# Optimization experiments

Hardware: AMD Instinct MI355X
Metric: run time of the kernel (lower is better)

Reference implementation:

```python
import jax, jax.numpy as jnp
import numpy as np

GAMMA = 1.0
BIG = 1e30  # finite stand-in for +inf (safe under logsumexp and autodiff)


def setup_inputs() -> dict:
    key = jax.random.key(0)
    kx, ky = jax.random.split(key)
    x = jax.random.normal(kx, (32, 512, 64), dtype=jnp.float32)
    y = jax.random.normal(ky, (32, 512, 64), dtype=jnp.float32)
    return {"x": x, "y": y}


def _cosine_dist(x, y):
    # 1 - cosine similarity; matches F.normalize(p=2, eps=1e-12)
    xn = x / jnp.maximum(jnp.linalg.norm(x, axis=-1, keepdims=True), 1e-12)
    yn = y / jnp.maximum(jnp.linalg.norm(y, axis=-1, keepdims=True), 1e-12)
    return 1.0 - jnp.einsum('btd,bsd->bts', xn, yn)


def _soft_dtw(D, gamma):
    # Anti-diagonal soft-DTW DP. D: [B, T1, T2] -> [B]
    B, T1, T2 = D.shape
    R0 = jnp.full((B, T1 + 1, T2 + 1), BIG, dtype=D.dtype).at[:, 0, 0].set(0.0)
    i = jnp.arange(1, T1 + 1)  # all rows; each diagonal k has j = k - i

    def step(R, k):
        j = k - i
        valid = (j >= 1) & (j <= T2)
        jc = jnp.where(valid, j, 0)  # clamp invalid lanes; masked below
        cost = jnp.where(valid, D[:, i - 1, jnp.clip(jc - 1, 0, T2 - 1)], 0.0)
        r_diag = R[:, i - 1, jnp.clip(jc - 1, 0, T2)]
        r_left = R[:, i, jnp.clip(jc - 1, 0, T2)]
        r_up = R[:, i - 1, jc]
        stacked = jnp.stack([r_diag, r_left, r_up], axis=0)  # [3, B, T1]
        stacked = jnp.where(valid[None, None, :], stacked, 0.0)
        soft_min = -gamma * jax.nn.logsumexp(-stacked / gamma, axis=0)
        new = cost + soft_min
        old = R[:, i, jc]
        R = R.at[:, i, jc].set(jnp.where(valid[None, :], new, old))
        return R, None

    ks = jnp.arange(2, T1 + T2 + 1)
    R, _ = jax.lax.scan(step, R0, ks)
    return R[:, T1, T2]


def reference(x, y):
    D_xy = _cosine_dist(x, y)
    D_xx = _cosine_dist(x, x)
    D_yy = _cosine_dist(y, y)
    sdtw_xy = _soft_dtw(D_xy, GAMMA)
    sdtw_xx = _soft_dtw(D_xx, GAMMA)
    sdtw_yy = _soft_dtw(D_yy, GAMMA)
    return sdtw_xy - 0.5 * (sdtw_xx + sdtw_yy)
```

## Files before the change

kernel.cpp:

```cpp
#include <hip/hip_runtime.h>
#include <hip/hip_fp16.h>

#define T1 512
#define NB 32
#define NP 96
#define DHEAD 64

#define RSLOTS 128
#define RBYTES (RSLOTS * 1024)
#define PFD 32

typedef __attribute__((ext_vector_type(8))) short bf16x8;
typedef __attribute__((ext_vector_type(4))) float f32x4;
typedef __attribute__((ext_vector_type(4))) unsigned int u32x4;

__global__ __launch_bounds__(256) void k_normalize(const float* __restrict__ x,
                                                   const float* __restrict__ y,
                                                   ushort* __restrict__ xb,
                                                   ushort* __restrict__ yb) {
  int wid  = threadIdx.x >> 6;
  int lane = threadIdx.x & 63;
  int row  = blockIdx.x * 4 + wid;
  const float* src; ushort* dst;
  if (row < NB * T1) { src = x + (size_t)row * DHEAD;            dst = xb + (size_t)row * DHEAD; }
  else { int r2 = row - NB * T1; src = y + (size_t)r2 * DHEAD;   dst = yb + (size_t)r2 * DHEAD; }
  float v = src[lane];
  float s = v * v;
  #pragma unroll
  for (int off = 32; off > 0; off >>= 1) s += __shfl_xor(s, off);
  float rn = 1.0f / fmaxf(sqrtf(s), 1e-12f);
  float o = v * rn;
  unsigned u = __float_as_uint(o);
  unsigned r = (u + 0x7fffu + ((u >> 16) & 1u)) >> 16;
  dst[lane] = (ushort)r;
}

__global__ __launch_bounds__(256) void k_gemm_w(const ushort* __restrict__ xb,
                                                const ushort* __restrict__ yb,
                                                __half* __restrict__ W) {
  __shared__ __attribute__((aligned(16))) __half blk[128][132];
  int pb = blockIdx.z;
  int p  = pb >> 5;
  int b  = pb & 31;
  const ushort* A  = ((p == 2) ? yb : xb) + (size_t)b * T1 * DHEAD;
  const ushort* Bm = ((p == 1) ? xb : yb) + (size_t)b * T1 * DHEAD;

  int wid = threadIdx.x >> 6, lane = threadIdx.x & 63;
  int wm = wid >> 1, wn = wid & 1;
  int i0b = blockIdx.x * 128, j0b = blockIdx.y * 128;
  int i0 = i0b + wm * 64;
  int j0 = j0b + wn * 64;
  int lr = lane & 15, kg = lane >> 4;

  f32x4 acc[4][4];
  #pragma unroll
  for (int ic = 0; ic < 4; ++ic)
    #pragma unroll
    for (int jc = 0; jc < 4; ++jc) acc[ic][jc] = (f32x4){0.f, 0.f, 0.f, 0.f};

  #pragma unroll
  for (int kk = 0; kk < 2; ++kk) {
    int ko = kk * 32 + kg * 8;
    bf16x8 af[4], bf[4];
    #pragma unroll
    for (int ic = 0; ic < 4; ++ic)
      af[ic] = *reinterpret_cast<const bf16x8*>(A + (size_t)(i0 + ic * 16 + lr) * DHEAD + ko);
    #pragma unroll
    for (int jc = 0; jc < 4; ++jc)
      bf[jc] = *reinterpret_cast<const bf16x8*>(Bm + (size_t)(j0 + jc * 16 + lr) * DHEAD + ko);
    #pragma unroll
    for (int ic = 0; ic < 4; ++ic)
      #pragma unroll
      for (int jc = 0; jc < 4; ++jc)
        acc[ic][jc] = __builtin_amdgcn_mfma_f32_16x16x32_bf16(af[ic], bf[jc], acc[ic][jc], 0, 0, 0);
  }

  const float NLOG2E = -1.44269504088896340736f;
  #pragma unroll
  for (int ic = 0; ic < 4; ++ic) {
    int il = wm * 64 + ic * 16 + (kg << 2);
    #pragma unroll
    for (int jc = 0; jc < 4; ++jc) {
      int jl = wn * 64 + jc * 16 + lr;
      union { __half h[4]; uint2 u; } pk;
      #pragma unroll
      for (int r = 0; r < 4; ++r) {
        float d = 1.0f - acc[ic][jc][r];
        pk.h[r] = __float2half(exp2f(NLOG2E * d));
      }
      *reinterpret_cast<uint2*>(&blk[jl][il]) = pk.u;
    }
  }
  __syncthreads();

  __half* Wp = W + (size_t)pb * (T1 * T1);
  int tr = threadIdx.x >> 4;
  int tc = threadIdx.x & 15;
  #pragma unroll
  for (int q = 0; q < 8; ++q) {
    int j = q * 16 + tr;
    u32x4 v = *reinterpret_cast<const u32x4*>(&blk[j][tc << 3]);
    *reinterpret_cast<u32x4*>(Wp + (size_t)(j0b + j) * T1 + i0b + (tc << 3)) = v;
  }
}

__global__ __launch_bounds__(64, 1) void k_dtw(const __half* __restrict__ W,
                                               float* __restrict__ res) {
  __shared__ __attribute__((aligned(16))) char ring[RBYTES];
  const int prob = blockIdx.x;
  const __half* Wp = W + (size_t)prob * (T1 * T1);
  const int lane = threadIdx.x;

  float Va[8], Vb[8];
  #pragma unroll
  for (int r = 0; r < 8; ++r) { Va[r] = 0.f; Vb[r] = 0.f; }
  float B2 = 0.f, B2p = 0.f;
  const float dgSeed = (lane == 0) ? 1.0f : 0.0f;

  auto dppshr = [](float v) -> float {
    return __int_as_float(__builtin_amdgcn_update_dpp(
        0, __float_as_int(v), 0x138 , 0xF, 0xF, true));
  };

#define SCALEBITS(dexp) __uint_as_float( \
    (unsigned)(127 + (int)fminf(fmaxf((dexp), -120.f), 120.f)) << 23)

  const char* gW = (const char*)Wp;
  const unsigned laneOff = (unsigned)(lane << 4);
  size_t colOff = (size_t)PFD << 10;
  unsigned lslot = (PFD << 10) & (RBYTES - 1);

  #pragma unroll
  for (int c = 0; c < PFD; ++c) {
    __builtin_amdgcn_global_load_lds(
        (const __attribute__((address_space(1))) void*)(gW + ((size_t)c << 10) + laneOff),
        (__attribute__((address_space(3))) void*)(ring + ((unsigned)(c << 10))), 16, 0, 0);
  }
  asm volatile("s_waitcnt vmcnt(24)" ::: "memory");

  u32x4 d0, d1, d2, d3, d4, d5, d6, d7;
  unsigned va0, va1, va2, va3, va4, va5, va6, va7;
#define RS_INIT(K) do { \
    d##K = *reinterpret_cast<const u32x4*>( \
        ring + ((((unsigned)(K - lane) & 127u) << 10) | (unsigned)(lane << 4))); \
    va##K = ((((unsigned)(8 + K - lane) & 127u) << 10) | (unsigned)(lane << 4)); \
  } while (0)
  RS_INIT(0); RS_INIT(1); RS_INIT(2); RS_INIT(3);
  RS_INIT(4); RS_INIT(5); RS_INIT(6); RS_INIT(7);
#undef RS_INIT

#define DTW_STEP(KK, BUF, VIN, VOUT, SDG, SEEDK, GUARD, RENORM) do {          \
    const int t_ = tb + (KK);                                                 \
    float nbUp_ = dppshr(VIN[7]);                    \
    float nbDg_ = dppshr(VOUT[7]);                   \
    float up_ = nbUp_ * sUp;                                                  \
    float dg_ = nbDg_ * (SDG);                                                \
    if (SEEDK) dg_ = dgSeed;                                                  \
    union { u32x4 u; __half h[8]; } cv_; cv_.u = d##BUF;                      \
    d##BUF = *reinterpret_cast<const u32x4*>(ring + va##BUF);   \
    va##BUF = (va##BUF + 8192u) & (RBYTES - 1);                               \
    __builtin_amdgcn_global_load_lds(                          \
        (const __attribute__((address_space(1))) void*)(gW + colOff + laneOff),\
        (__attribute__((address_space(3))) void*)(ring + lslot), 16, 0, 0);   \
    lslot = (lslot + 1024u) & (RBYTES - 1);                                   \
    colOff += ((t_ + PFD) < (T1 - 1)) ? 1024 : 0;  \
    float wv_[8];                                                             \
    _Pragma("unroll")                                                         \
    for (int r = 0; r < 8; ++r) wv_[r] = __half2float(cv_.h[r]);              \
    bool act_ = true;                                                         \
    if (GUARD) { int j_ = t_ - lane; act_ = ((unsigned)j_ < (unsigned)T1); }  \
    if (act_) {                                                               \
      float c_ = fmaf(wv_[0], up_, wv_[0] * (dg_ + VIN[0]));                  \
      VOUT[0] = c_;                                                           \
      _Pragma("unroll")                                                       \
      for (int r = 1; r < 8; ++r) {                                           \
        c_ = fmaf(wv_[r], c_, wv_[r] * (VIN[r-1] + VIN[r]));                  \
        VOUT[r] = c_;                                                         \
      }                                                                       \
      if (RENORM) {                            \
        float m_ = fmaxf(fmaxf(fmaxf(VOUT[0],VOUT[1]),fmaxf(VOUT[2],VOUT[3])),\
                         fmaxf(fmaxf(VOUT[4],VOUT[5]),fmaxf(VOUT[6],VOUT[7])));\
        int e_ = (int)((__float_as_uint(m_) >> 23) & 0xFF) - 127;             \
        e_ = e_ < -126 ? -126 : (e_ > 126 ? 126 : e_);                        \
        float sc_ = __uint_as_float((unsigned)(127 - e_) << 23);              \
        _Pragma("unroll")                                                     \
        for (int r = 0; r < 8; ++r) VOUT[r] *= sc_;                           \
        B2p = B2; B2 -= (float)e_;                                            \
      }                                                                       \
    }                                                                         \
  } while (0)

#define DTW_GROUP(GUARD, SEED) do {                                           \
    asm volatile("s_waitcnt vmcnt(16)" ::: "memory");      \
    float nbBn_ = dppshr(B2);                 \
    float nbBo_ = dppshr(B2p);                \
    float sUp  = SCALEBITS(B2 - nbBn_);                                       \
    float sDg0 = SCALEBITS(B2 - nbBo_);                                       \
    DTW_STEP(0,  0, Va, Vb, sDg0, SEED,  GUARD, false);                       \
    DTW_STEP(1,  1, Vb, Va, sUp,  false, GUARD, false);                       \
    DTW_STEP(2,  2, Va, Vb, sUp,  false, GUARD, false);                       \
    DTW_STEP(3,  3, Vb, Va, sUp,  false, GUARD, false);                       \
    DTW_STEP(4,  4, Va, Vb, sUp,  false, GUARD, false);                       \
    DTW_STEP(5,  5, Vb, Va, sUp,  false, GUARD, false);                       \
    DTW_STEP(6,  6, Va, Vb, sUp,  false, GUARD, false);                       \
    DTW_STEP(7,  7, Vb, Va, sUp,  false, GUARD, false);                       \
    asm volatile("s_waitcnt vmcnt(16)" ::: "memory");      \
    DTW_STEP(8,  0, Va, Vb, sUp,  false, GUARD, false);                       \
    DTW_STEP(9,  1, Vb, Va, sUp,  false, GUARD, false);                       \
    DTW_STEP(10, 2, Va, Vb, sUp,  false, GUARD, false);                       \
    DTW_STEP(11, 3, Vb, Va, sUp,  false, GUARD, false);                       \
    DTW_STEP(12, 4, Va, Vb, sUp,  false, GUARD, false);                       \
    DTW_STEP(13, 5, Vb, Va, sUp,  false, GUARD, false);                       \
    DTW_STEP(14, 6, Va, Vb, sUp,  false, GUARD, false);                       \
    DTW_STEP(15, 7, Vb, Va, sUp,  false, GUARD, true);                        \
  } while (0)

  { const int tb = 0; DTW_GROUP(true, true); }
  #pragma unroll 1
  for (int tb = 16; tb < 64; tb += 16)   DTW_GROUP(true,  false);
  #pragma unroll 1
  for (int tb = 64; tb < 560; tb += 16)  DTW_GROUP(false, false);
  { const int tb = 560; DTW_GROUP(true, false); }

  if (lane == 63) {
    res[prob] = (B2 - log2f(Vb[7])) * 0.69314718055994530942f;
  }
#undef DTW_STEP
#undef DTW_GROUP
#undef SCALEBITS
}

__global__ void k_combine(const float* __restrict__ res, float* __restrict__ out) {
  int b = threadIdx.x;
  if (b < NB) out[b] = res[b] - 0.5f * (res[NB + b] + res[2 * NB + b]);
}

extern "C" void kernel_launch(void* const* d_in, const int* in_sizes, int n_in,
                              void* d_out, int out_size, void* d_ws, size_t ws_size,
                              hipStream_t stream) {
  const float* x = (const float*)d_in[0];
  const float* y = (const float*)d_in[1];
  float* out = (float*)d_out;

  const size_t xb_off  = 0;
  const size_t yb_off  = (size_t)NB * T1 * DHEAD * sizeof(ushort);
  const size_t W_off   = 2 * yb_off;
  const size_t res_off = W_off + (size_t)3 * NB * T1 * T1 * sizeof(__half);
  const size_t need    = res_off + NP * sizeof(float);

  if (ws_size < need) {
    hipMemsetAsync(d_out, 0xFF, (size_t)out_size * sizeof(float), stream);
    return;
  }

  ushort* xb  = (ushort*)((char*)d_ws + xb_off);
  ushort* yb  = (ushort*)((char*)d_ws + yb_off);
  __half* W   = (__half*)((char*)d_ws + W_off);
  float*  res = (float*)((char*)d_ws + res_off);

  hipLaunchKernelGGL(k_normalize, dim3(8192), dim3(256), 0, stream, x, y, xb, yb);
  hipLaunchKernelGGL(k_gemm_w, dim3(4, 4, 96), dim3(256), 0, stream, xb, yb, W);
  hipLaunchKernelGGL(k_dtw, dim3(NP), dim3(64), 0, stream, W, res);
  hipLaunchKernelGGL(k_combine, dim3(1), dim3(64), 0, stream, res, out);
}
```

Measured before the change: 84.30 us.

## Process two DTW columns per lane step, halving wavefront sweep length

Each DTW step now computes two consecutive columns per lane, so each lane covers 16 rows per tile (lane offset 2*lane). The number of anti-diagonal steps drops from about 576 to about 320, with fewer DPP shuffles and waitcnt barriers per column. The LDS ring is resized to 152 slots with a prefetch depth of 30, and two global-to-LDS loads are issued per step. In exchange each step has a longer dependent FMA chain and more registers are live, and the ring indexing becomes harder to verify.

```diff
diff --git a/kernel.cpp b/kernel.cpp
--- a/kernel.cpp
+++ b/kernel.cpp
@@ -6,9 +6,9 @@
 #define NP 96
 #define DHEAD 64
 
-#define RSLOTS 128
+#define RSLOTS 152
 #define RBYTES (RSLOTS * 1024)
-#define PFD 32
+#define PFD 30
 
 typedef __attribute__((ext_vector_type(8))) short bf16x8;
 typedef __attribute__((ext_vector_type(4))) float f32x4;
@@ -115,6 +115,7 @@
   #pragma unroll
   for (int r = 0; r < 8; ++r) { Va[r] = 0.f; Vb[r] = 0.f; }
   float B2 = 0.f, B2p = 0.f;
+  float m7 = 0.f, d7 = 0.f;
   const float dgSeed = (lane == 0) ? 1.0f : 0.0f;
 
   auto dppshr = [](float v) -> float {
@@ -125,109 +126,136 @@
 #define SCALEBITS(dexp) __uint_as_float( \
     (unsigned)(127 + (int)fminf(fmaxf((dexp), -120.f), 120.f)) << 23)
 
+#define GLL16(GP, LP) __builtin_amdgcn_global_load_lds( \
+    (const __attribute__((address_space(1))) void*)(GP), \
+    (__attribute__((address_space(3))) void*)(LP), 16, 0, 0)
+
   const char* gW = (const char*)Wp;
   const unsigned laneOff = (unsigned)(lane << 4);
-  size_t colOff = (size_t)PFD << 10;
-  unsigned lslot = (PFD << 10) & (RBYTES - 1);
-
-  #pragma unroll
-  for (int c = 0; c < PFD; ++c) {
-    __builtin_amdgcn_global_load_lds(
-        (const __attribute__((address_space(1))) void*)(gW + ((size_t)c << 10) + laneOff),
-        (__attribute__((address_space(3))) void*)(ring + ((unsigned)(c << 10))), 16, 0, 0);
-  }
-  asm volatile("s_waitcnt vmcnt(24)" ::: "memory");
-
-  u32x4 d0, d1, d2, d3, d4, d5, d6, d7;
+
+  #pragma unroll
+  for (int c = 0; c < PFD; ++c)
+    GLL16(gW + ((size_t)c << 10) + laneOff, ring + ((unsigned)(c << 10)));
+  asm volatile("s_waitcnt vmcnt(22)" ::: "memory");
+
+  u32x4 d0, d1, d2, d3, d4, d5, d6, d7b;
   unsigned va0, va1, va2, va3, va4, va5, va6, va7;
-#define RS_INIT(K) do { \
-    d##K = *reinterpret_cast<const u32x4*>( \
-        ring + ((((unsigned)(K - lane) & 127u) << 10) | (unsigned)(lane << 4))); \
-    va##K = ((((unsigned)(8 + K - lane) & 127u) << 10) | (unsigned)(lane << 4)); \
+#define RS_INIT(K, DN) do { \
+    int n_ = (K) - 2 * lane; unsigned s_ = (unsigned)(n_ < 0 ? n_ + RSLOTS : n_); \
+    DN = *reinterpret_cast<const u32x4*>(ring + (s_ << 10) + laneOff); \
+    int m_ = n_ + 8; unsigned sm_ = (unsigned)(m_ < 0 ? m_ + RSLOTS : m_); \
+    va##K = (sm_ << 10) + laneOff; \
   } while (0)
-  RS_INIT(0); RS_INIT(1); RS_INIT(2); RS_INIT(3);
-  RS_INIT(4); RS_INIT(5); RS_INIT(6); RS_INIT(7);
+  RS_INIT(0, d0); RS_INIT(1, d1); RS_INIT(2, d2); RS_INIT(3, d3);
+  RS_INIT(4, d4); RS_INIT(5, d5); RS_INIT(6, d6); RS_INIT(7, d7b);
 #undef RS_INIT
 
-#define DTW_STEP(KK, BUF, VIN, VOUT, SDG, SEEDK, GUARD, RENORM) do {          \
+  unsigned colA = PFD, colB = PFD + 1;
+  unsigned slA = (unsigned)(PFD << 10);
+  unsigned slB = (unsigned)((PFD + 1) << 10);
+
+#define DTW_STEP2(KK, DA, DB, SM, SD, SEEDK, GUARD) do {                      \
     const int t_ = tb + (KK);                                                 \
-    float nbUp_ = dppshr(VIN[7]);                    \
-    float nbDg_ = dppshr(VOUT[7]);                   \
-    float up_ = nbUp_ * sUp;                                                  \
-    float dg_ = nbDg_ * (SDG);                                                \
-    if (SEEDK) dg_ = dgSeed;                                                  \
-    union { u32x4 u; __half h[8]; } cv_; cv_.u = d##BUF;                      \
-    d##BUF = *reinterpret_cast<const u32x4*>(ring + va##BUF);   \
-    va##BUF = (va##BUF + 8192u) & (RBYTES - 1);                               \
-    __builtin_amdgcn_global_load_lds(                          \
-        (const __attribute__((address_space(1))) void*)(gW + colOff + laneOff),\
-        (__attribute__((address_space(3))) void*)(ring + lslot), 16, 0, 0);   \
-    lslot = (lslot + 1024u) & (RBYTES - 1);                                   \
-    colOff += ((t_ + PFD) < (T1 - 1)) ? 1024 : 0;  \
-    float wv_[8];                                                             \
+    float nbLive_ = dppshr(Va[7]);                 \
+    float nbMid_  = dppshr(m7);                \
+    float nbDel_  = dppshr(d7);                    \
+    d7 = Va[7];                                     \
+    float up0_ = nbMid_ * (SM);                                               \
+    float dg0_ = nbDel_ * (SD);                                               \
+    float up1_ = nbLive_ * sUp;                                               \
+    if (SEEDK) dg0_ = dgSeed;                \
+    union { u32x4 u; __half h[8]; } cA_; cA_.u = DA;                          \
+    union { u32x4 u; __half h[8]; } cB_; cB_.u = DB;                          \
+    float wA_[8], wB_[8];                                                     \
     _Pragma("unroll")                                                         \
-    for (int r = 0; r < 8; ++r) wv_[r] = __half2float(cv_.h[r]);              \
+    for (int r = 0; r < 8; ++r) { wA_[r] = __half2float(cA_.h[r]);            \
+                                  wB_[r] = __half2float(cB_.h[r]); }          \
+    DA = *reinterpret_cast<const u32x4*>(ring + va##KK##A_IDX);               \
+    va##KK##A_IDX += 8192u; if (va##KK##A_IDX >= RBYTES) va##KK##A_IDX -= RBYTES; \
+    DB = *reinterpret_cast<const u32x4*>(ring + va##KK##B_IDX);               \
+    va##KK##B_IDX += 8192u; if (va##KK##B_IDX >= RBYTES) va##KK##B_IDX -= RBYTES; \
+    { unsigned cAc_ = colA > 511u ? 511u : colA;                              \
+      unsigned cBc_ = colB > 511u ? 511u : colB;                              \
+      GLL16(gW + ((size_t)cAc_ << 10) + laneOff, ring + slA);                 \
+      GLL16(gW + ((size_t)cBc_ << 10) + laneOff, ring + slB);                 \
+      colA += 2u; colB += 2u;                                                 \
+      slA += 2048u; if (slA >= RBYTES) slA -= RBYTES;                         \
+      slB += 2048u; if (slB >= RBYTES) slB -= RBYTES; }                       \
     bool act_ = true;                                                         \
-    if (GUARD) { int j_ = t_ - lane; act_ = ((unsigned)j_ < (unsigned)T1); }  \
+    if (GUARD) { unsigned u_ = (unsigned)(t_ - lane); act_ = (u_ <= 255u); }  \
     if (act_) {                                                               \
-      float c_ = fmaf(wv_[0], up_, wv_[0] * (dg_ + VIN[0]));                  \
-      VOUT[0] = c_;                                                           \
+      float c_ = fmaf(wA_[0], up0_, wA_[0] * (dg0_ + Va[0]));  Vb[0] = c_;    \
       _Pragma("unroll")                                                       \
       for (int r = 1; r < 8; ++r) {                                           \
-        c_ = fmaf(wv_[r], c_, wv_[r] * (VIN[r-1] + VIN[r]));                  \
-        VOUT[r] = c_;                                                         \
+        c_ = fmaf(wA_[r], c_, wA_[r] * (Va[r-1] + Va[r]));  Vb[r] = c_;       \
       }                                                                       \
-      if (RENORM) {                            \
-        float m_ = fmaxf(fmaxf(fmaxf(VOUT[0],VOUT[1]),fmaxf(VOUT[2],VOUT[3])),\
-                         fmaxf(fmaxf(VOUT[4],VOUT[5]),fmaxf(VOUT[6],VOUT[7])));\
-        int e_ = (int)((__float_as_uint(m_) >> 23) & 0xFF) - 127;             \
+      m7 = Vb[7];                               \
+      c_ = fmaf(wB_[0], up1_, wB_[0] * (up0_ + Vb[0]));  Va[0] = c_;          \
+      _Pragma("unroll")                                                       \
+      for (int r = 1; r < 8; ++r) {                                           \
+        c_ = fmaf(wB_[r], c_, wB_[r] * (Vb[r-1] + Vb[r]));  Va[r] = c_;       \
+      }                                                                       \
+      if ((KK) == 7) {                        \
+        float mx_ = fmaxf(fmaxf(fmaxf(Va[0],Va[1]),fmaxf(Va[2],Va[3])),       \
+                          fmaxf(fmaxf(Va[4],Va[5]),fmaxf(Va[6],Va[7])));      \
+        int e_ = (int)((__float_as_uint(mx_) >> 23) & 0xFF) - 127;            \
         e_ = e_ < -126 ? -126 : (e_ > 126 ? 126 : e_);                        \
         float sc_ = __uint_as_float((unsigned)(127 - e_) << 23);              \
         _Pragma("unroll")                                                     \
-        for (int r = 0; r < 8; ++r) VOUT[r] *= sc_;                           \
+        for (int r = 0; r < 8; ++r) Va[r] *= sc_;                             \
         B2p = B2; B2 -= (float)e_;                                            \
       }                                                                       \
     }                                                                         \
   } while (0)
 
-#define DTW_GROUP(GUARD, SEED) do {                                           \
-    asm volatile("s_waitcnt vmcnt(16)" ::: "memory");      \
-    float nbBn_ = dppshr(B2);                 \
-    float nbBo_ = dppshr(B2p);                \
+#define va0A_IDX va0
+#define va0B_IDX va1
+#define va1A_IDX va2
+#define va1B_IDX va3
+#define va2A_IDX va4
+#define va2B_IDX va5
+#define va3A_IDX va6
+#define va3B_IDX va7
+#define va4A_IDX va0
+#define va4B_IDX va1
+#define va5A_IDX va2
+#define va5B_IDX va3
+#define va6A_IDX va4
+#define va6B_IDX va5
+#define va7A_IDX va6
+#define va7B_IDX va7
+
+#define DTW_GROUP2(GUARD, SEED) do {                                          \
+    asm volatile("s_waitcnt vmcnt(14)" ::: "memory");     \
+    float nbBn_ = dppshr(B2);                                                 \
+    float nbBo_ = dppshr(B2p);                                                \
     float sUp  = SCALEBITS(B2 - nbBn_);                                       \
     float sDg0 = SCALEBITS(B2 - nbBo_);                                       \
-    DTW_STEP(0,  0, Va, Vb, sDg0, SEED,  GUARD, false);                       \
-    DTW_STEP(1,  1, Vb, Va, sUp,  false, GUARD, false);                       \
-    DTW_STEP(2,  2, Va, Vb, sUp,  false, GUARD, false);                       \
-    DTW_STEP(3,  3, Vb, Va, sUp,  false, GUARD, false);                       \
-    DTW_STEP(4,  4, Va, Vb, sUp,  false, GUARD, false);                       \
-    DTW_STEP(5,  5, Vb, Va, sUp,  false, GUARD, false);                       \
-    DTW_STEP(6,  6, Va, Vb, sUp,  false, GUARD, false);                       \
-    DTW_STEP(7,  7, Vb, Va, sUp,  false, GUARD, false);                       \
-    asm volatile("s_waitcnt vmcnt(16)" ::: "memory");      \
-    DTW_STEP(8,  0, Va, Vb, sUp,  false, GUARD, false);                       \
-    DTW_STEP(9,  1, Vb, Va, sUp,  false, GUARD, false);                       \
-    DTW_STEP(10, 2, Va, Vb, sUp,  false, GUARD, false);                       \
-    DTW_STEP(11, 3, Vb, Va, sUp,  false, GUARD, false);                       \
-    DTW_STEP(12, 4, Va, Vb, sUp,  false, GUARD, false);                       \
-    DTW_STEP(13, 5, Vb, Va, sUp,  false, GUARD, false);                       \
-    DTW_STEP(14, 6, Va, Vb, sUp,  false, GUARD, false);                       \
-    DTW_STEP(15, 7, Vb, Va, sUp,  false, GUARD, true);                        \
+    DTW_STEP2(0, d0,  d1,  sDg0, sDg0, SEED,  GUARD);                         \
+    DTW_STEP2(1, d2,  d3,  sUp,  sUp,  false, GUARD);                         \
+    DTW_STEP2(2, d4,  d5,  sUp,  sUp,  false, GUARD);                         \
+    DTW_STEP2(3, d6,  d7b, sUp,  sUp,  false, GUARD);                         \
+    asm volatile("s_waitcnt vmcnt(14)" ::: "memory");     \
+    DTW_STEP2(4, d0,  d1,  sUp,  sUp,  false, GUARD);                         \
+    DTW_STEP2(5, d2,  d3,  sUp,  sUp,  false, GUARD);                         \
+    DTW_STEP2(6, d4,  d5,  sUp,  sUp,  false, GUARD);                         \
+    DTW_STEP2(7, d6,  d7b, sUp,  sUp,  false, GUARD);                         \
   } while (0)
 
-  { const int tb = 0; DTW_GROUP(true, true); }
+  { const int tb = 0; DTW_GROUP2(true, true); }
   #pragma unroll 1
-  for (int tb = 16; tb < 64; tb += 16)   DTW_GROUP(true,  false);
+  for (int tb = 8; tb < 64; tb += 8)    DTW_GROUP2(true,  false);
   #pragma unroll 1
-  for (int tb = 64; tb < 560; tb += 16)  DTW_GROUP(false, false);
-  { const int tb = 560; DTW_GROUP(true, false); }
+  for (int tb = 64; tb < 312; tb += 8)  DTW_GROUP2(false, false);
+  { const int tb = 312; DTW_GROUP2(true, false); }
 
   if (lane == 63) {
-    res[prob] = (B2 - log2f(Vb[7])) * 0.69314718055994530942f;
-  }
-#undef DTW_STEP
-#undef DTW_GROUP
+    res[prob] = (B2 - log2f(Va[7])) * 0.69314718055994530942f;
+  }
+#undef DTW_STEP2
+#undef DTW_GROUP2
 #undef SCALEBITS
+#undef GLL16
 }
 
 __global__ void k_combine(const float* __restrict__ res, float* __restrict__ out) {
```

Result: slower. 93.90 us (+11.4%).

## Fuse normalization into GEMM via LDS and fold combine into DTW atomics

Applied to the files above, without the earlier changes.

Drops the separate normalize kernel. Each GEMM block now loads its fp32 x/y tiles, L2-normalizes them, converts to bf16 into shared memory, and feeds the MFMA fragments from LDS. The final combine kernel is also removed: the DTW blocks atomically add their signed contributions into the output, which is zeroed first with a memset. This saves launches and the bf16 staging round trip. In exchange, each row is normalized redundantly by four column blocks, LDS usage rises, and the summation order becomes nondeterministic.

```diff
diff --git a/kernel.cpp b/kernel.cpp
--- a/kernel.cpp
+++ b/kernel.cpp
@@ -14,42 +14,44 @@
 typedef __attribute__((ext_vector_type(4))) float f32x4;
 typedef __attribute__((ext_vector_type(4))) unsigned int u32x4;
 
-__global__ __launch_bounds__(256) void k_normalize(const float* __restrict__ x,
-                                                   const float* __restrict__ y,
-                                                   ushort* __restrict__ xb,
-                                                   ushort* __restrict__ yb) {
-  int wid  = threadIdx.x >> 6;
-  int lane = threadIdx.x & 63;
-  int row  = blockIdx.x * 4 + wid;
-  const float* src; ushort* dst;
-  if (row < NB * T1) { src = x + (size_t)row * DHEAD;            dst = xb + (size_t)row * DHEAD; }
-  else { int r2 = row - NB * T1; src = y + (size_t)r2 * DHEAD;   dst = yb + (size_t)r2 * DHEAD; }
-  float v = src[lane];
-  float s = v * v;
-  #pragma unroll
-  for (int off = 32; off > 0; off >>= 1) s += __shfl_xor(s, off);
-  float rn = 1.0f / fmaxf(sqrtf(s), 1e-12f);
-  float o = v * rn;
-  unsigned u = __float_as_uint(o);
-  unsigned r = (u + 0x7fffu + ((u >> 16) & 1u)) >> 16;
-  dst[lane] = (ushort)r;
-}
-
-__global__ __launch_bounds__(256) void k_gemm_w(const ushort* __restrict__ xb,
-                                                const ushort* __restrict__ yb,
+__global__ __launch_bounds__(256) void k_gemm_w(const float* __restrict__ x,
+                                                const float* __restrict__ y,
                                                 __half* __restrict__ W) {
   __shared__ __attribute__((aligned(16))) __half blk[128][132];
+  __shared__ __attribute__((aligned(16))) ushort xnL[128][72];
+  __shared__ __attribute__((aligned(16))) ushort ynL[128][72];
   int pb = blockIdx.z;
   int p  = pb >> 5;
   int b  = pb & 31;
-  const ushort* A  = ((p == 2) ? yb : xb) + (size_t)b * T1 * DHEAD;
-  const ushort* Bm = ((p == 1) ? xb : yb) + (size_t)b * T1 * DHEAD;
+  int i0b = blockIdx.x * 128, j0b = blockIdx.y * 128;
+  const float* Asrc = ((p == 2) ? y : x) + (size_t)b * T1 * DHEAD + (size_t)i0b * DHEAD;
+  const float* Bsrc = ((p == 1) ? x : y) + (size_t)b * T1 * DHEAD + (size_t)j0b * DHEAD;
 
   int wid = threadIdx.x >> 6, lane = threadIdx.x & 63;
+
+  #pragma unroll 1
+  for (int r = wid; r < 128; r += 4) {
+    float v = Asrc[(size_t)r * DHEAD + lane];
+    float s = v * v;
+    #pragma unroll
+    for (int off = 32; off > 0; off >>= 1) s += __shfl_xor(s, off);
+    float o = v * (1.0f / fmaxf(sqrtf(s), 1e-12f));
+    unsigned u = __float_as_uint(o);
+    xnL[r][lane] = (ushort)((u + 0x7fffu + ((u >> 16) & 1u)) >> 16);
+  }
+  #pragma unroll 1
+  for (int r = wid; r < 128; r += 4) {
+    float v = Bsrc[(size_t)r * DHEAD + lane];
+    float s = v * v;
+    #pragma unroll
+    for (int off = 32; off > 0; off >>= 1) s += __shfl_xor(s, off);
+    float o = v * (1.0f / fmaxf(sqrtf(s), 1e-12f));
+    unsigned u = __float_as_uint(o);
+    ynL[r][lane] = (ushort)((u + 0x7fffu + ((u >> 16) & 1u)) >> 16);
+  }
+  __syncthreads();
+
   int wm = wid >> 1, wn = wid & 1;
-  int i0b = blockIdx.x * 128, j0b = blockIdx.y * 128;
-  int i0 = i0b + wm * 64;
-  int j0 = j0b + wn * 64;
   int lr = lane & 15, kg = lane >> 4;
 
   f32x4 acc[4][4];
@@ -64,10 +66,10 @@
     bf16x8 af[4], bf[4];
     #pragma unroll
     for (int ic = 0; ic < 4; ++ic)
-      af[ic] = *reinterpret_cast<const bf16x8*>(A + (size_t)(i0 + ic * 16 + lr) * DHEAD + ko);
+      af[ic] = *reinterpret_cast<const bf16x8*>(&xnL[wm * 64 + ic * 16 + lr][ko]);
     #pragma unroll
     for (int jc = 0; jc < 4; ++jc)
-      bf[jc] = *reinterpret_cast<const bf16x8*>(Bm + (size_t)(j0 + jc * 16 + lr) * DHEAD + ko);
+      bf[jc] = *reinterpret_cast<const bf16x8*>(&ynL[wn * 64 + jc * 16 + lr][ko]);
     #pragma unroll
     for (int ic = 0; ic < 4; ++ic)
       #pragma unroll
@@ -105,7 +107,7 @@
 }
 
 __global__ __launch_bounds__(64, 1) void k_dtw(const __half* __restrict__ W,
-                                               float* __restrict__ res) {
+                                               float* __restrict__ out) {
   __shared__ __attribute__((aligned(16))) char ring[RBYTES];
   const int prob = blockIdx.x;
   const __half* Wp = W + (size_t)prob * (T1 * T1);
@@ -223,16 +225,13 @@
   { const int tb = 560; DTW_GROUP(true, false); }
 
   if (lane == 63) {
-    res[prob] = (B2 - log2f(Vb[7])) * 0.69314718055994530942f;
+    float val = (B2 - log2f(Vb[7])) * 0.69314718055994530942f;
+    float coeff = (prob < 32) ? 1.0f : -0.5f;
+    atomicAdd(out + (prob & 31), coeff * val);
   }
 #undef DTW_STEP
 #undef DTW_GROUP
 #undef SCALEBITS
-}
-
-__global__ void k_combine(const float* __restrict__ res, float* __restrict__ out) {
-  int b = threadIdx.x;
-  if (b < NB) out[b] = res[b] - 0.5f * (res[NB + b] + res[2 * NB + b]);
 }
 
 extern "C" void kernel_launch(void* const* d_in, const int* in_sizes, int n_in,
@@ -242,24 +241,14 @@
   const float* y = (const float*)d_in[1];
   float* out = (float*)d_out;
 
-  const size_t xb_off  = 0;
-  const size_t yb_off  = (size_t)NB * T1 * DHEAD * sizeof(ushort);
-  const size_t W_off   = 2 * yb_off;
-  const size_t res_off = W_off + (size_t)3 * NB * T1 * T1 * sizeof(__half);
-  const size_t need    = res_off + NP * sizeof(float);
-
+  const size_t need = (size_t)3 * NB * T1 * T1 * sizeof(__half);
   if (ws_size < need) {
     hipMemsetAsync(d_out, 0xFF, (size_t)out_size * sizeof(float), stream);
     return;
   }
-
-  ushort* xb  = (ushort*)((char*)d_ws + xb_off);
-  ushort* yb  = (ushort*)((char*)d_ws + yb_off);
-  __half* W   = (__half*)((char*)d_ws + W_off);
-  float*  res = (float*)((char*)d_ws + res_off);
-
-  hipLaunchKernelGGL(k_normalize, dim3(8192), dim3(256), 0, stream, x, y, xb, yb);
-  hipLaunchKernelGGL(k_gemm_w, dim3(4, 4, 96), dim3(256), 0, stream, xb, yb, W);
-  hipLaunchKernelGGL(k_dtw, dim3(NP), dim3(64), 0, stream, W, res);
-  hipLaunchKernelGGL(k_combine, dim3(1), dim3(64), 0, stream, res, out);
+  __half* W = (__half*)d_ws;
+
+  hipMemsetAsync(d_out, 0, (size_t)out_size * sizeof(float), stream);
+  hipLaunchKernelGGL(k_gemm_w, dim3(4, 4, 96), dim3(256), 0, stream, x, y, W);
+  hipLaunchKernelGGL(k_dtw, dim3(NP), dim3(64), 0, stream, W, out);
 }
```

After: 176.9 us. +109.9%, slower.
